# Optimization experiments

Hardware: AMD Instinct MI355X
Metric: run time of the kernel (lower is better)

Reference implementation:

```python
import jax, jax.numpy as jnp
import numpy as np

HIDDEN = 512
ATT = 512
B, S = 32, 2048


def setup_inputs() -> dict:
    key = jax.random.key(0)
    ks = jax.random.split(key, 9)
    enc_output = jax.random.normal(ks[0], (B, S, 2 * HIDDEN), dtype=jnp.float32)
    decoder_hidden = jax.random.normal(ks[1], (B, HIDDEN), dtype=jnp.float32)
    masks = jax.random.randint(ks[2], (B, S, 1), 0, 2).astype(jnp.bool_)
    # Learned params (init_weights style: uniform(-0.1, 0.1), zero bias)
    W_enc = jax.random.uniform(ks[3], (2 * HIDDEN, ATT), minval=-0.1, maxval=0.1, dtype=jnp.float32)
    b_enc = jnp.zeros((ATT,), dtype=jnp.float32)
    W_dec = jax.random.uniform(ks[4], (HIDDEN, ATT), minval=-0.1, maxval=0.1, dtype=jnp.float32)
    b_dec = jnp.zeros((ATT,), dtype=jnp.float32)
    W_att = jax.random.uniform(ks[5], (ATT, 1), minval=-0.1, maxval=0.1, dtype=jnp.float32)
    b_att = jnp.zeros((1,), dtype=jnp.float32)
    return {
        "enc_output": enc_output,
        "decoder_hidden": decoder_hidden,
        "masks": masks,
        "W_enc": W_enc,
        "b_enc": b_enc,
        "W_dec": W_dec,
        "b_dec": b_dec,
        "W_att": W_att,
        "b_att": b_att,
    }


def reference(enc_output, decoder_hidden, masks, W_enc, b_enc, W_dec, b_dec, W_att, b_att):
    # encoder_att: [B, S, A]
    encoder_att = jnp.einsum("bse,ea->bsa", enc_output, W_enc) + b_enc
    # decoder_att: [B, A]
    decoder_att = decoder_hidden @ W_dec + b_dec
    # scores: [B, S, 1]
    scores = jnp.tanh(encoder_att + decoder_att[:, None, :]) @ W_att + b_att
    scores = jnp.where(masks, -jnp.inf, scores)
    att_weights = jax.nn.softmax(scores, axis=1)  # softmax over seq dim
    # context over encoder_att (note: original weights encoder_att, not enc_output)
    att_context_vector = jnp.sum(encoder_att * att_weights, axis=1)  # [B, A]
    return att_context_vector
```

## Files before the change

kernel.cpp:

```cpp
#include <hip/hip_runtime.h>
#include <math.h>

#define B_  32
#define S_  2048
#define E_  1024
#define A_  512
#define H_  512

#define MB   64
#define NCH  (S_ / MB)
#define KT   32

typedef __bf16 bf16;
typedef __attribute__((ext_vector_type(8))) __bf16 bf16x8;
typedef __attribute__((ext_vector_type(4))) __bf16 bf16x4;
typedef __attribute__((ext_vector_type(4))) float  f32x4;

typedef const __attribute__((address_space(1))) unsigned int g_u32;
typedef __attribute__((address_space(3))) unsigned int lds_u32;

__device__ __forceinline__ void glds16(const void* g, void* l) {
    __builtin_amdgcn_global_load_lds((g_u32*)g, (lds_u32*)l, 16, 0, 0);
}

__device__ __forceinline__ float fast_tanh(float x) {
    x = fminf(fmaxf(x, -15.f), 15.f);
    const float e = __expf(2.f * x);
    return (e - 1.f) / (e + 1.f);
}

__global__ __launch_bounds__(256)
void wsplit_kernel(const float* __restrict__ Wenc,
                   bf16* __restrict__ Whi, bf16* __restrict__ Wlo,
                   float* __restrict__ dec_att) {
    const int idx = blockIdx.x * 256 + threadIdx.x;
    if (idx < B_ * A_) dec_att[idx] = 0.f;
    const int k = idx >> 9;
    const int a = idx & 511;
    const float x = Wenc[idx];
    const bf16 h = (bf16)x;
    const float r = x - (float)h;
    const bf16 l = (bf16)r;
    Whi[(size_t)a * E_ + k] = h;
    Wlo[(size_t)a * E_ + k] = l;
}

__global__ __launch_bounds__(256)
void dec_att_kernel(const float* __restrict__ dh,
                    const float* __restrict__ Wdec,
                    const float* __restrict__ bdec,
                    float* __restrict__ dec_att) {
    __shared__ float dhl[64];
    const int b   = blockIdx.x >> 3;
    const int seg = blockIdx.x & 7;
    const int t   = threadIdx.x;
    if (t < 64) dhl[t] = dh[b * H_ + seg * 64 + t];
    __syncthreads();
    const int a0 = t, a1 = t + 256;
    float acc0 = 0.f, acc1 = 0.f;
    const float* Wrow = Wdec + (size_t)(seg * 64) * A_;
#pragma unroll 8
    for (int h = 0; h < 64; ++h) {
        const float s = dhl[h];
        acc0 += s * Wrow[h * A_ + a0];
        acc1 += s * Wrow[h * A_ + a1];
    }
    if (seg == 0) { acc0 += bdec[a0]; acc1 += bdec[a1]; }
    atomicAdd(&dec_att[b * A_ + a0], acc0);
    atomicAdd(&dec_att[b * A_ + a1], acc1);
}

__global__ __launch_bounds__(512, 4)
void fused_kernel(const float* __restrict__ enc,
                  const int*   __restrict__ masks,
                  const bf16*  __restrict__ Whi_g,
                  const bf16*  __restrict__ Wlo_g,
                  const float* __restrict__ benc,
                  const float* __restrict__ Watt,
                  const float* __restrict__ batt,
                  const float* __restrict__ dec_att,
                  float* __restrict__ pm,
                  float* __restrict__ pl,
                  float* __restrict__ pctx) {
    __shared__ union {
        struct {
            bf16 Whi[A_ * KT];
            bf16 Wlo[A_ * KT];
        } w;
        struct {
            float red[MB * 128];
            float decl[A_];
            float wattl[A_];
            float bencl[A_];
            float redb[512];
            float red2[A_ * 4];
        } e;
    } sm;
    __shared__ __align__(16) bf16 Ahi[MB * KT];
    __shared__ __align__(16) bf16 Alo[MB * KT];
    __shared__ float score_s[MB];
    __shared__ float p_s[MB];
    __shared__ int   mask_s[MB];

    const int t    = threadIdx.x;
    const int wv   = t >> 6;
    const int L    = t & 63;
    const int quad = L >> 4;
    const int colL = L & 15;
    const int b    = blockIdx.x >> 5;
    const int ch   = blockIdx.x & 31;
    const int s0   = ch * MB;

    const float* encB = enc + ((size_t)(b * S_ + s0)) * E_;

    f32x4 acc[4][4];
#pragma unroll
    for (int mt = 0; mt < 4; ++mt)
#pragma unroll
        for (int nt = 0; nt < 4; ++nt) acc[mt][nt] = (f32x4){0.f, 0.f, 0.f, 0.f};

    const int arow  = t >> 3;
    const int akq   = t & 7;
    const int a_dst = ((arow >> 4) * 512) + (((akq >> 1) * 16 + (arow & 15)) * 8)
                      + (akq & 1) * 4;
    const size_t a_src_row = (size_t)arow * E_ + akq * 4;

    for (int kt = 0; kt < E_ / KT; ++kt) {
        const int k0 = kt * KT;
        const float4 av = *(const float4*)(encB + a_src_row + k0);

        __syncthreads();

#pragma unroll
        for (int i = 0; i < 4; ++i) {
            const int I = wv * 4 + i;
            const size_t goff = (size_t)(I * 16 + colL) * E_ + k0 + quad * 8;
            glds16(Whi_g + goff, &sm.w.Whi[I * 512]);
            glds16(Wlo_g + goff, &sm.w.Wlo[I * 512]);
        }

        {
            const bf16 h0 = (bf16)av.x, h1 = (bf16)av.y, h2 = (bf16)av.z, h3 = (bf16)av.w;
            const bf16 l0 = (bf16)(av.x - (float)h0);
            const bf16 l1 = (bf16)(av.y - (float)h1);
            const bf16 l2 = (bf16)(av.z - (float)h2);
            const bf16 l3 = (bf16)(av.w - (float)h3);
            bf16x4 hv; hv[0] = h0; hv[1] = h1; hv[2] = h2; hv[3] = h3;
            bf16x4 lv; lv[0] = l0; lv[1] = l1; lv[2] = l2; lv[3] = l3;
            *(bf16x4*)&Ahi[a_dst] = hv;
            *(bf16x4*)&Alo[a_dst] = lv;
        }

        __syncthreads();

        {
            bf16x8 bb[4];
#pragma unroll
            for (int nt = 0; nt < 4; ++nt)
                bb[nt] = *(const bf16x8*)&sm.w.Whi[(wv * 4 + nt) * 512 + L * 8];
#pragma unroll
            for (int mt = 0; mt < 4; ++mt) {
                const bf16x8 ah = *(const bf16x8*)&Ahi[mt * 512 + L * 8];
                const bf16x8 al = *(const bf16x8*)&Alo[mt * 512 + L * 8];
#pragma unroll
                for (int nt = 0; nt < 4; ++nt) {
                    acc[mt][nt] = __builtin_amdgcn_mfma_f32_16x16x32_bf16(ah, bb[nt], acc[mt][nt], 0, 0, 0);
                    acc[mt][nt] = __builtin_amdgcn_mfma_f32_16x16x32_bf16(al, bb[nt], acc[mt][nt], 0, 0, 0);
                }
            }
        }
        {
            bf16x8 bb[4];
#pragma unroll
            for (int nt = 0; nt < 4; ++nt)
                bb[nt] = *(const bf16x8*)&sm.w.Wlo[(wv * 4 + nt) * 512 + L * 8];
#pragma unroll
            for (int mt = 0; mt < 4; ++mt) {
                const bf16x8 ah = *(const bf16x8*)&Ahi[mt * 512 + L * 8];
#pragma unroll
                for (int nt = 0; nt < 4; ++nt)
                    acc[mt][nt] = __builtin_amdgcn_mfma_f32_16x16x32_bf16(ah, bb[nt], acc[mt][nt], 0, 0, 0);
            }
        }
    }

    __syncthreads();

    {
        sm.e.decl[t]  = dec_att[b * A_ + t];
        sm.e.wattl[t] = Watt[t];
        sm.e.bencl[t] = benc[t];
        if (t < MB) mask_s[t] = masks[(size_t)b * S_ + s0 + t];
    }
    __syncthreads();

    float sp[4][4];
#pragma unroll
    for (int mt = 0; mt < 4; ++mt)
#pragma unroll
        for (int r = 0; r < 4; ++r) sp[mt][r] = 0.f;

#pragma unroll
    for (int nt = 0; nt < 4; ++nt) {
        const int cg = wv * 64 + nt * 16 + colL;
        const float bv  = sm.e.bencl[cg];
        const float dv  = sm.e.decl[cg];
        const float wav = sm.e.wattl[cg];
#pragma unroll
        for (int mt = 0; mt < 4; ++mt)
#pragma unroll
            for (int r = 0; r < 4; ++r) {
                const float ea = acc[mt][nt][r] + bv;
                acc[mt][nt][r] = ea;
                sp[mt][r] += fast_tanh(ea + dv) * wav;
            }
    }
#pragma unroll
    for (int mt = 0; mt < 4; ++mt)
#pragma unroll
        for (int r = 0; r < 4; ++r) {
            const int row = mt * 16 + quad * 4 + r;
            sm.e.red[row * 128 + wv * 16 + colL] = sp[mt][r];
        }
    __syncthreads();

    {
        const int r = t >> 3, seg = t & 7;
        float s = 0.f;
#pragma unroll
        for (int j = 0; j < 16; ++j) s += sm.e.red[r * 128 + seg * 16 + j];
        sm.e.redb[r * 8 + seg] = s;
    }
    __syncthreads();
    if (t < MB) {
        float s = 0.f;
#pragma unroll
        for (int j = 0; j < 8; ++j) s += sm.e.redb[t * 8 + j];
        score_s[t] = s + batt[0];
    }
    __syncthreads();

    float m_loc = -1e30f;
    for (int r = 0; r < MB; ++r)
        if (!mask_s[r]) m_loc = fmaxf(m_loc, score_s[r]);
    if (t < MB) p_s[t] = mask_s[t] ? 0.f : __expf(score_s[t] - m_loc);
    __syncthreads();

    float ctxl[4] = {0.f, 0.f, 0.f, 0.f};
#pragma unroll
    for (int mt = 0; mt < 4; ++mt)
#pragma unroll
        for (int r = 0; r < 4; ++r) {
            const float p = p_s[mt * 16 + quad * 4 + r];
#pragma unroll
            for (int nt = 0; nt < 4; ++nt) ctxl[nt] += p * acc[mt][nt][r];
        }
#pragma unroll
    for (int nt = 0; nt < 4; ++nt) {
        const int cg = wv * 64 + nt * 16 + colL;
        sm.e.red2[cg * 4 + quad] = ctxl[nt];
    }
    __syncthreads();

    {
        const float c = sm.e.red2[t * 4] + sm.e.red2[t * 4 + 1] +
                        sm.e.red2[t * 4 + 2] + sm.e.red2[t * 4 + 3];
        pctx[(size_t)blockIdx.x * A_ + t] = c;
    }
    if (t == 0) {
        float l = 0.f;
        for (int r = 0; r < MB; ++r) l += p_s[r];
        pm[blockIdx.x] = m_loc;
        pl[blockIdx.x] = l;
    }
}

__global__ __launch_bounds__(512)
void combine_kernel(const float* __restrict__ pm,
                    const float* __restrict__ pl,
                    const float* __restrict__ pctx,
                    float* __restrict__ out) {
    const int b = blockIdx.x;
    const int t = threadIdx.x;
    float m_g = -1e30f;
    for (int c = 0; c < NCH; ++c) m_g = fmaxf(m_g, pm[b * NCH + c]);
    float L = 0.f;
    for (int c = 0; c < NCH; ++c)
        L += pl[b * NCH + c] * __expf(pm[b * NCH + c] - m_g);
    const float inv = 1.f / L;
    float s = 0.f;
    for (int c = 0; c < NCH; ++c)
        s += pctx[((size_t)b * NCH + c) * A_ + t] * __expf(pm[b * NCH + c] - m_g);
    out[b * A_ + t] = s * inv;
}

extern "C" void kernel_launch(void* const* d_in, const int* in_sizes, int n_in,
                              void* d_out, int out_size, void* d_ws, size_t ws_size,
                              hipStream_t stream) {
    const float* enc  = (const float*)d_in[0];
    const float* dh   = (const float*)d_in[1];
    const int*   mks  = (const int*)  d_in[2];
    const float* Wenc = (const float*)d_in[3];
    const float* benc = (const float*)d_in[4];
    const float* Wdec = (const float*)d_in[5];
    const float* bdec = (const float*)d_in[6];
    const float* Watt = (const float*)d_in[7];
    const float* batt = (const float*)d_in[8];
    float* out = (float*)d_out;

    float* ws      = (float*)d_ws;
    float* dec_att = ws;
    float* pm      = dec_att + B_ * A_;
    float* pl      = pm + B_ * NCH;
    float* pctx    = pl + B_ * NCH;
    bf16*  Whi     = (bf16*)(pctx + B_ * NCH * A_);
    bf16*  Wlo     = Whi + (size_t)A_ * E_;
    (void)in_sizes; (void)n_in; (void)out_size; (void)ws_size;

    wsplit_kernel<<<(E_ * A_) / 256, 256, 0, stream>>>(Wenc, Whi, Wlo, dec_att);
    dec_att_kernel<<<B_ * 8, 256, 0, stream>>>(dh, Wdec, bdec, dec_att);
    fused_kernel<<<B_ * NCH, 512, 0, stream>>>(
        enc, mks, Whi, Wlo, benc, Watt, batt, dec_att, pm, pl, pctx);
    combine_kernel<<<B_, 512, 0, stream>>>(pm, pl, pctx, out);
}
```

Before: 643.0 us.

## Double M tile, prefetch encoder loads, swizzle LDS, shuffle reductions, tiled W split

The per-block sequence tile grows from 64 to 128 rows, so each staged W_enc k-slice feeds twice as many MFMAs and the grid halves to 512 blocks at 2 blocks per CU. The next k-step's encoder data is prefetched into registers, the A tile is stored with an XOR-swizzled LDS layout, and the score and context reductions use wave shuffles in place of LDS round trips. The weight split kernel now transposes through a shared-memory tile so its global writes are coalesced. In exchange the larger accumulator raises register pressure and lowers occupancy.

```diff
diff --git a/kernel.cpp b/kernel.cpp
--- a/kernel.cpp
+++ b/kernel.cpp
@@ -7,13 +7,13 @@
 #define A_  512
 #define H_  512
 
-#define MB   64
+#define MB   128
 #define NCH  (S_ / MB)
 #define KT   32
+#define NK   (E_ / KT)
 
 typedef __bf16 bf16;
 typedef __attribute__((ext_vector_type(8))) __bf16 bf16x8;
-typedef __attribute__((ext_vector_type(4))) __bf16 bf16x4;
 typedef __attribute__((ext_vector_type(4))) float  f32x4;
 
 typedef const __attribute__((address_space(1))) unsigned int g_u32;
@@ -33,16 +33,40 @@
 void wsplit_kernel(const float* __restrict__ Wenc,
                    bf16* __restrict__ Whi, bf16* __restrict__ Wlo,
                    float* __restrict__ dec_att) {
-    const int idx = blockIdx.x * 256 + threadIdx.x;
-    if (idx < B_ * A_) dec_att[idx] = 0.f;
-    const int k = idx >> 9;
-    const int a = idx & 511;
-    const float x = Wenc[idx];
-    const bf16 h = (bf16)x;
-    const float r = x - (float)h;
-    const bf16 l = (bf16)r;
-    Whi[(size_t)a * E_ + k] = h;
-    Wlo[(size_t)a * E_ + k] = l;
+    __shared__ float tile[64][65];
+    const int t  = threadIdx.x;
+    const int kb = blockIdx.x >> 3;
+    const int ab = blockIdx.x & 7;
+    const int k0 = kb * 64, a0 = ab * 64;
+
+    const int di = blockIdx.x * 256 + t;
+    if (di < B_ * A_) dec_att[di] = 0.f;
+
+#pragma unroll
+    for (int p = 0; p < 8; ++p) {
+        const int kk = p * 8 + (t >> 5);
+        const int aa = (t & 31) * 2;
+        const float2 v = *(const float2*)&Wenc[(size_t)(k0 + kk) * A_ + a0 + aa];
+        tile[kk][aa]     = v.x;
+        tile[kk][aa + 1] = v.y;
+    }
+    __syncthreads();
+
+    const int aa  = t >> 2;
+    const int kk0 = (t & 3) * 16;
+    bf16x8 hv0, hv1, lv0, lv1;
+#pragma unroll
+    for (int j = 0; j < 16; ++j) {
+        const float x = tile[kk0 + j][aa];
+        const bf16 h = (bf16)x;
+        const bf16 l = (bf16)(x - (float)h);
+        if (j < 8) { hv0[j] = h; lv0[j] = l; }
+        else       { hv1[j - 8] = h; lv1[j - 8] = l; }
+    }
+    bf16* dh_ = Whi + (size_t)(a0 + aa) * E_ + k0 + kk0;
+    bf16* dl_ = Wlo + (size_t)(a0 + aa) * E_ + k0 + kk0;
+    *(bf16x8*)dh_ = hv0; *((bf16x8*)dh_ + 1) = hv1;
+    *(bf16x8*)dl_ = lv0; *((bf16x8*)dl_ + 1) = lv1;
 }
 
 __global__ __launch_bounds__(256)
@@ -70,7 +94,7 @@
     atomicAdd(&dec_att[b * A_ + a1], acc1);
 }
 
-__global__ __launch_bounds__(512, 4)
+__global__ __launch_bounds__(512, 2)
 void fused_kernel(const float* __restrict__ enc,
                   const int*   __restrict__ masks,
                   const bf16*  __restrict__ Whi_g,
@@ -82,24 +106,13 @@
                   float* __restrict__ pm,
                   float* __restrict__ pl,
                   float* __restrict__ pctx) {
-    __shared__ union {
-        struct {
-            bf16 Whi[A_ * KT];
-            bf16 Wlo[A_ * KT];
-        } w;
-        struct {
-            float red[MB * 128];
-            float decl[A_];
-            float wattl[A_];
-            float bencl[A_];
-            float redb[512];
-            float red2[A_ * 4];
-        } e;
-    } sm;
-    __shared__ __align__(16) bf16 Ahi[MB * KT];
-    __shared__ __align__(16) bf16 Alo[MB * KT];
-    __shared__ float score_s[MB];
-    __shared__ float p_s[MB];
+    __shared__ __align__(16) bf16 Whi_s[A_ * KT];
+    __shared__ __align__(16) bf16 Wlo_s[A_ * KT];
+    __shared__ __align__(16) bf16 Ahi_s[MB * KT];
+    __shared__ __align__(16) bf16 Alo_s[MB * KT];
+    __shared__ float decl[A_], wattl[A_], bencl[A_];
+    __shared__ float red[MB * 8];
+    __shared__ float score_s[MB], p_s[MB];
     __shared__ int   mask_s[MB];
 
     const int t    = threadIdx.x;
@@ -107,107 +120,101 @@
     const int L    = t & 63;
     const int quad = L >> 4;
     const int colL = L & 15;
-    const int b    = blockIdx.x >> 5;
-    const int ch   = blockIdx.x & 31;
+    const int b    = blockIdx.x >> 4;
+    const int ch   = blockIdx.x & 15;
     const int s0   = ch * MB;
 
     const float* encB = enc + ((size_t)(b * S_ + s0)) * E_;
 
-    f32x4 acc[4][4];
-#pragma unroll
-    for (int mt = 0; mt < 4; ++mt)
+    f32x4 acc[8][4];
+#pragma unroll
+    for (int mt = 0; mt < 8; ++mt)
 #pragma unroll
         for (int nt = 0; nt < 4; ++nt) acc[mt][nt] = (f32x4){0.f, 0.f, 0.f, 0.f};
 
-    const int arow  = t >> 3;
-    const int akq   = t & 7;
-    const int a_dst = ((arow >> 4) * 512) + (((akq >> 1) * 16 + (arow & 15)) * 8)
-                      + (akq & 1) * 4;
-    const size_t a_src_row = (size_t)arow * E_ + akq * 4;
-
-    for (int kt = 0; kt < E_ / KT; ++kt) {
+    const int arow = t >> 2;
+    const int akq  = t & 3;
+    const int a_wr = ((arow >> 4) * 512) + akq * 128 +
+                     (((arow & 15) ^ (akq << 2)) * 8);
+    const float* aptr = encB + (size_t)arow * E_ + akq * 8;
+    const int a_rd = quad * 128 + (((L & 15) ^ (quad << 2)) * 8);
+
+    float4 cvA = *(const float4*)(aptr);
+    float4 cvB = *(const float4*)(aptr + 4);
+
+    for (int kt = 0; kt < NK; ++kt) {
         const int k0 = kt * KT;
-        const float4 av = *(const float4*)(encB + a_src_row + k0);
-
         __syncthreads();
 
 #pragma unroll
         for (int i = 0; i < 4; ++i) {
             const int I = wv * 4 + i;
             const size_t goff = (size_t)(I * 16 + colL) * E_ + k0 + quad * 8;
-            glds16(Whi_g + goff, &sm.w.Whi[I * 512]);
-            glds16(Wlo_g + goff, &sm.w.Wlo[I * 512]);
+            glds16(Whi_g + goff, &Whi_s[I * 512]);
+            glds16(Wlo_g + goff, &Wlo_s[I * 512]);
         }
 
         {
-            const bf16 h0 = (bf16)av.x, h1 = (bf16)av.y, h2 = (bf16)av.z, h3 = (bf16)av.w;
-            const bf16 l0 = (bf16)(av.x - (float)h0);
-            const bf16 l1 = (bf16)(av.y - (float)h1);
-            const bf16 l2 = (bf16)(av.z - (float)h2);
-            const bf16 l3 = (bf16)(av.w - (float)h3);
-            bf16x4 hv; hv[0] = h0; hv[1] = h1; hv[2] = h2; hv[3] = h3;
-            bf16x4 lv; lv[0] = l0; lv[1] = l1; lv[2] = l2; lv[3] = l3;
-            *(bf16x4*)&Ahi[a_dst] = hv;
-            *(bf16x4*)&Alo[a_dst] = lv;
+            const float xs[8] = {cvA.x, cvA.y, cvA.z, cvA.w,
+                                 cvB.x, cvB.y, cvB.z, cvB.w};
+            bf16x8 hv, lv;
+#pragma unroll
+            for (int j = 0; j < 8; ++j) {
+                const bf16 h = (bf16)xs[j];
+                hv[j] = h;
+                lv[j] = (bf16)(xs[j] - (float)h);
+            }
+            *(bf16x8*)&Ahi_s[a_wr] = hv;
+            *(bf16x8*)&Alo_s[a_wr] = lv;
         }
 
         __syncthreads();
 
-        {
-            bf16x8 bb[4];
-#pragma unroll
-            for (int nt = 0; nt < 4; ++nt)
-                bb[nt] = *(const bf16x8*)&sm.w.Whi[(wv * 4 + nt) * 512 + L * 8];
-#pragma unroll
-            for (int mt = 0; mt < 4; ++mt) {
-                const bf16x8 ah = *(const bf16x8*)&Ahi[mt * 512 + L * 8];
-                const bf16x8 al = *(const bf16x8*)&Alo[mt * 512 + L * 8];
-#pragma unroll
-                for (int nt = 0; nt < 4; ++nt) {
-                    acc[mt][nt] = __builtin_amdgcn_mfma_f32_16x16x32_bf16(ah, bb[nt], acc[mt][nt], 0, 0, 0);
-                    acc[mt][nt] = __builtin_amdgcn_mfma_f32_16x16x32_bf16(al, bb[nt], acc[mt][nt], 0, 0, 0);
-                }
+        if (kt + 1 < NK) {
+            const float* np = aptr + (kt + 1) * KT;
+            cvA = *(const float4*)(np);
+            cvB = *(const float4*)(np + 4);
+        }
+
+        bf16x8 bh[4], bl[4];
+#pragma unroll
+        for (int nt = 0; nt < 4; ++nt) {
+            bh[nt] = *(const bf16x8*)&Whi_s[(wv * 4 + nt) * 512 + L * 8];
+            bl[nt] = *(const bf16x8*)&Wlo_s[(wv * 4 + nt) * 512 + L * 8];
+        }
+#pragma unroll
+        for (int mt = 0; mt < 8; ++mt) {
+            const bf16x8 ah = *(const bf16x8*)&Ahi_s[mt * 512 + a_rd];
+            const bf16x8 al = *(const bf16x8*)&Alo_s[mt * 512 + a_rd];
+#pragma unroll
+            for (int nt = 0; nt < 4; ++nt) {
+                acc[mt][nt] = __builtin_amdgcn_mfma_f32_16x16x32_bf16(ah, bh[nt], acc[mt][nt], 0, 0, 0);
+                acc[mt][nt] = __builtin_amdgcn_mfma_f32_16x16x32_bf16(al, bh[nt], acc[mt][nt], 0, 0, 0);
+                acc[mt][nt] = __builtin_amdgcn_mfma_f32_16x16x32_bf16(ah, bl[nt], acc[mt][nt], 0, 0, 0);
             }
         }
-        {
-            bf16x8 bb[4];
-#pragma unroll
-            for (int nt = 0; nt < 4; ++nt)
-                bb[nt] = *(const bf16x8*)&sm.w.Wlo[(wv * 4 + nt) * 512 + L * 8];
-#pragma unroll
-            for (int mt = 0; mt < 4; ++mt) {
-                const bf16x8 ah = *(const bf16x8*)&Ahi[mt * 512 + L * 8];
-#pragma unroll
-                for (int nt = 0; nt < 4; ++nt)
-                    acc[mt][nt] = __builtin_amdgcn_mfma_f32_16x16x32_bf16(ah, bb[nt], acc[mt][nt], 0, 0, 0);
-            }
-        }
-    }
-
-    __syncthreads();
-
-    {
-        sm.e.decl[t]  = dec_att[b * A_ + t];
-        sm.e.wattl[t] = Watt[t];
-        sm.e.bencl[t] = benc[t];
-        if (t < MB) mask_s[t] = masks[(size_t)b * S_ + s0 + t];
-    }
-    __syncthreads();
-
-    float sp[4][4];
-#pragma unroll
-    for (int mt = 0; mt < 4; ++mt)
+    }
+
+    decl[t < A_ ? t : 0]  = dec_att[b * A_ + (t < A_ ? t : 0)];
+    wattl[t] = Watt[t];
+    bencl[t] = benc[t];
+    if (t < MB) mask_s[t] = masks[(size_t)b * S_ + s0 + t];
+    __syncthreads();
+
+    float sp[8][4];
+#pragma unroll
+    for (int mt = 0; mt < 8; ++mt)
 #pragma unroll
         for (int r = 0; r < 4; ++r) sp[mt][r] = 0.f;
 
 #pragma unroll
     for (int nt = 0; nt < 4; ++nt) {
         const int cg = wv * 64 + nt * 16 + colL;
-        const float bv  = sm.e.bencl[cg];
-        const float dv  = sm.e.decl[cg];
-        const float wav = sm.e.wattl[cg];
-#pragma unroll
-        for (int mt = 0; mt < 4; ++mt)
+        const float bv  = bencl[cg];
+        const float dv  = decl[cg];
+        const float wav = wattl[cg];
+#pragma unroll
+        for (int mt = 0; mt < 8; ++mt)
 #pragma unroll
             for (int r = 0; r < 4; ++r) {
                 const float ea = acc[mt][nt][r] + bv;
@@ -216,26 +223,25 @@
             }
     }
 #pragma unroll
-    for (int mt = 0; mt < 4; ++mt)
-#pragma unroll
-        for (int r = 0; r < 4; ++r) {
-            const int row = mt * 16 + quad * 4 + r;
-            sm.e.red[row * 128 + wv * 16 + colL] = sp[mt][r];
-        }
-    __syncthreads();
-
-    {
-        const int r = t >> 3, seg = t & 7;
-        float s = 0.f;
-#pragma unroll
-        for (int j = 0; j < 16; ++j) s += sm.e.red[r * 128 + seg * 16 + j];
-        sm.e.redb[r * 8 + seg] = s;
-    }
-    __syncthreads();
+    for (int d = 1; d < 16; d <<= 1)
+#pragma unroll
+        for (int mt = 0; mt < 8; ++mt)
+#pragma unroll
+            for (int r = 0; r < 4; ++r)
+                sp[mt][r] += __shfl_xor(sp[mt][r], d);
+    if (colL == 0) {
+#pragma unroll
+        for (int mt = 0; mt < 8; ++mt)
+#pragma unroll
+            for (int r = 0; r < 4; ++r)
+                red[(mt * 16 + quad * 4 + r) * 8 + wv] = sp[mt][r];
+    }
+    __syncthreads();
+
     if (t < MB) {
         float s = 0.f;
 #pragma unroll
-        for (int j = 0; j < 8; ++j) s += sm.e.redb[t * 8 + j];
+        for (int j = 0; j < 8; ++j) s += red[t * 8 + j];
         score_s[t] = s + batt[0];
     }
     __syncthreads();
@@ -248,7 +254,7 @@
 
     float ctxl[4] = {0.f, 0.f, 0.f, 0.f};
 #pragma unroll
-    for (int mt = 0; mt < 4; ++mt)
+    for (int mt = 0; mt < 8; ++mt)
 #pragma unroll
         for (int r = 0; r < 4; ++r) {
             const float p = p_s[mt * 16 + quad * 4 + r];
@@ -257,15 +263,13 @@
         }
 #pragma unroll
     for (int nt = 0; nt < 4; ++nt) {
-        const int cg = wv * 64 + nt * 16 + colL;
-        sm.e.red2[cg * 4 + quad] = ctxl[nt];
-    }
-    __syncthreads();
-
-    {
-        const float c = sm.e.red2[t * 4] + sm.e.red2[t * 4 + 1] +
-                        sm.e.red2[t * 4 + 2] + sm.e.red2[t * 4 + 3];
-        pctx[(size_t)blockIdx.x * A_ + t] = c;
+        ctxl[nt] += __shfl_xor(ctxl[nt], 16);
+        ctxl[nt] += __shfl_xor(ctxl[nt], 32);
+    }
+    if (quad == 0) {
+#pragma unroll
+        for (int nt = 0; nt < 4; ++nt)
+            pctx[(size_t)blockIdx.x * A_ + wv * 64 + nt * 16 + colL] = ctxl[nt];
     }
     if (t == 0) {
         float l = 0.f;
@@ -317,7 +321,7 @@
     bf16*  Wlo     = Whi + (size_t)A_ * E_;
     (void)in_sizes; (void)n_in; (void)out_size; (void)ws_size;
 
-    wsplit_kernel<<<(E_ * A_) / 256, 256, 0, stream>>>(Wenc, Whi, Wlo, dec_att);
+    wsplit_kernel<<<128, 256, 0, stream>>>(Wenc, Whi, Wlo, dec_att);
     dec_att_kernel<<<B_ * 8, 256, 0, stream>>>(dh, Wdec, bdec, dec_att);
     fused_kernel<<<B_ * NCH, 512, 0, stream>>>(
         enc, mks, Whi, Wlo, benc, Watt, batt, dec_att, pm, pl, pctx);
```

Measured after the change: 581.4 us. -9.6%, faster.
